# Performance work log

Measured on AMD Instinct MI355X. Metric: run time of the kernel, lower is better.

Reference implementation:

```python
import math
import jax, jax.numpy as jnp
import numpy as np

L_MAX = 3
PADDED = (1, 1, 2, 3)            # padded_l_list
K_MAX_L = (128, 96, 64, 32)      # channel bounds per l
FEATS = (32, 32, 32, 32)         # k_max_l[l] - k_max_l[l+1]
N_ATOMS = 20000
N_EDGES = 80000
N_RADIAL = 32
HIDDEN = 128
EPS = 1e-6


def setup_inputs() -> dict:
    key = jax.random.key(0)
    ks = jax.random.split(key, 40)
    it = iter(range(40))
    nk = lambda: ks[next(it)]
    inp = {}
    inp['rb'] = jax.random.normal(nk(), (L_MAX + 1, N_EDGES, N_RADIAL), jnp.float32)
    for l in range(L_MAX + 1):
        inp[f'sh{l}'] = jax.random.normal(nk(), (N_EDGES, 2 * l + 1), jnp.float32)
    for l in range(L_MAX + 1):
        P = PADDED[l]
        inp[f'f{l}'] = jax.random.normal(nk(), (N_ATOMS, P + 1, P + 1, FEATS[l]), jnp.float32)
    for P in (1, 2, 3):
        n = (P + 1) ** 2
        inp[f'U{P}'] = jax.random.normal(nk(), (n, n), jnp.float32) / math.sqrt(n)
    inp['gammas'] = jnp.ones((L_MAX + 1, 32), jnp.float32)
    inp['Win'] = jax.random.normal(nk(), (L_MAX + 1, 32, 32), jnp.float32) / math.sqrt(32.0)
    inp['Wout'] = jax.random.normal(nk(), (L_MAX + 1, 32, 32), jnp.float32) / math.sqrt(32.0)
    inp['A'] = jax.random.normal(nk(), (L_MAX + 1, N_RADIAL, HIDDEN), jnp.float32) / math.sqrt(float(N_RADIAL))
    for l in range(L_MAX + 1):
        inp[f'B{l}'] = jax.random.normal(nk(), (HIDDEN, K_MAX_L[l]), jnp.float32) / math.sqrt(float(HIDDEN))
    inp['msg_scale'] = jnp.float32(0.5)
    inp['centers'] = jax.random.randint(nk(), (N_EDGES,), 0, N_ATOMS)
    inp['neighbors'] = jax.random.randint(nk(), (N_EDGES,), 0, N_ATOMS)
    return inp


def _forward(rb, shs, feats, Us, gammas, Win, Wout, A, Bs, msg_scale, centers, neighbors):
    n_atoms = feats[0].shape[0]
    # EquivariantRMSNorm (norm over uncoupled i,j indices per channel) + linear_in
    h = []
    for l in range(L_MAX + 1):
        f = feats[l]
        rms = jnp.sqrt(jnp.mean(f * f, axis=(1, 2), keepdims=True) + EPS)
        fn = (f / rms) * gammas[l]
        h.append(jnp.einsum('nijf,fg->nijg', fn, Win[l]))
    # per-l radial MLP: [E, n_radial] -> silu -> [E, k_max_l[l]]
    rbm = [jax.nn.silu(rb[l] @ A[l]) @ Bs[l] for l in range(L_MAX + 1)]
    # vector expansion [E, 2l+1, k_max_l[l]]
    vexp = [shs[l][:, :, None] * rbm[l][:, None, :] for l in range(L_MAX + 1)]
    # split channels into per-l groups, uncouple via CG matrix U
    unc = []
    for l in range(L_MAX + 1):
        lower = K_MAX_L[l + 1] if l < L_MAX else 0
        upper = K_MAX_L[l]
        group = [vexp[lp][:, :, lower:upper] for lp in range(l + 1)]
        P = PADDED[l]
        if len(group) < P + 1:
            group.append(jnp.zeros((N_EDGES, 2 * P + 1, upper - lower), group[0].dtype))
        stacked = jnp.concatenate(group, axis=1)  # [E, (P+1)^2, feat]
        u = jnp.einsum('pq,eqf->epf', Us[P], stacked)
        unc.append(u.reshape(N_EDGES, P + 1, P + 1, upper - lower))
    # gather -> per-l tensor product -> scatter-add -> linear_out -> residual
    out = []
    for l in range(L_MAX + 1):
        P = PADDED[l]
        msg = jnp.einsum('eijf,ejkf->eikf', unc[l], h[l][neighbors]) / math.sqrt(P + 1.0)
        pooled = jnp.zeros((n_atoms,) + msg.shape[1:], msg.dtype).at[centers].add(msg) * msg_scale
        out.append(feats[l] + jnp.einsum('nijf,fg->nijg', pooled, Wout[l]))
    return tuple(out)


def reference(rb, sh0, sh1, sh2, sh3, f0, f1, f2, f3, U1, U2, U3, gammas, Win, Wout, A, B0, B1, B2, B3, msg_scale, centers, neighbors):
    return _forward(rb, [sh0, sh1, sh2, sh3], [f0, f1, f2, f3], {1: U1, 2: U2, 3: U3}, gammas, Win, Wout, A, [B0, B1, B2, B3], msg_scale, centers, neighbors)
```

## Files before the change

### kernel.cpp

```cpp
#include <hip/hip_runtime.h>
#include <cstdint>

#define NA 20000
#define NE 80000

typedef __attribute__((ext_vector_type(8))) short short8;
typedef __attribute__((ext_vector_type(4))) float f32x4;
typedef unsigned short ushort_t;

constexpr int HOFFc[4]   = {0, 2560000, 5120000, 10880000};
constexpr int RBMOFFc[4] = {0, 128, 224, 288};

__device__ __forceinline__ ushort_t f2bf(float x) {
    union { float f; unsigned u; } v; v.f = x;
    unsigned r = v.u + 0x7fffu + ((v.u >> 16) & 1u);
    return (ushort_t)(r >> 16);
}
__device__ __forceinline__ float bf2f(ushort_t u) {
    union { unsigned u; float f; } v; v.u = ((unsigned)u) << 16;
    return v.f;
}
__device__ __forceinline__ unsigned pack2(float a, float b) {
    return ((unsigned)f2bf(b) << 16) | (unsigned)f2bf(a);
}

__global__ __launch_bounds__(256)
void k_hist_prep(const int* __restrict__ centers, int* __restrict__ counts,
                 const float* __restrict__ B0, const float* __restrict__ B1,
                 const float* __restrict__ B2, const float* __restrict__ B3,
                 const float* __restrict__ A, const float* __restrict__ Win,
                 ushort_t* __restrict__ BT, ushort_t* __restrict__ ATb,
                 ushort_t* __restrict__ WinTb)
{
    const int b = blockIdx.x;
    if (b < 313) {
        const int e = b * 256 + threadIdx.x;
        if (e < NE) atomicAdd(&counts[centers[e]], 1);
        return;
    }
    const int i = (b - 313) * 256 + threadIdx.x;
    if (i < 40960) {
        const int n = i >> 7, k = i & 127;
        const float* src; int nl, N;
        if (n < 128)      { src = B0; nl = n;       N = 128; }
        else if (n < 224) { src = B1; nl = n - 128; N = 96;  }
        else if (n < 288) { src = B2; nl = n - 224; N = 64;  }
        else              { src = B3; nl = n - 288; N = 32;  }
        BT[i] = f2bf(src[k * N + nl]);
    } else if (i < 57344) {
        const int j2 = i - 40960;
        const int l = j2 >> 12, rem = j2 & 4095, jrow = rem >> 5, k = rem & 31;
        ATb[j2] = f2bf(A[l * 4096 + k * 128 + jrow]);
    } else if (i < 61440) {
        const int j3 = i - 57344;
        const int l = j3 >> 10, rem = j3 & 1023, g = rem >> 5, k = rem & 31;
        WinTb[j3] = f2bf(Win[l * 1024 + k * 32 + g]);
    }
}

template<int S, int AB>
__device__ __forceinline__ void norm_body(
    const float* __restrict__ fsel, const float* __restrict__ gammas, int l,
    const ushort_t* __restrict__ WinTb, ushort_t* __restrict__ hb,
    ushort_t* __restrict__ s_wt, float* __restrict__ s_scale)
{
    const int t = threadIdx.x;
    const int na0 = blockIdx.x * AB;

    if (t < 128) {
        reinterpret_cast<uint4*>(s_wt)[t] =
            reinterpret_cast<const uint4*>(WinTb + l * 1024)[t];
    }
    for (int i = t; i < AB * 32; i += 256) {
        const int a = i >> 5, c = i & 31;
        int aa = na0 + a; if (aa > NA - 1) aa = NA - 1;
        const float* fp = fsel + ((size_t)aa * S) * 32 + c;
        float ss = 0.f;
        #pragma unroll
        for (int s = 0; s < S; ++s) { const float v = fp[s * 32]; ss += v * v; }
        s_scale[i] = gammas[l * 32 + c] * rsqrtf(ss / (float)S + 1e-6f);
    }
    __syncthreads();

    const int w = t >> 6, lane = t & 63, l15 = lane & 15, lg = lane >> 4;
    const int row = w * 16 + l15;
    const bool rvalid = row < AB * S;
    const int rowc = rvalid ? row : 0;
    const int a = rowc / S, s = rowc % S;
    const int atom = na0 + a;
    const bool store_ok = rvalid && (atom < NA);
    const int atomc = (atom < NA) ? atom : (NA - 1);

    const float* fp = fsel + ((size_t)atomc * S + s) * 32 + lg * 8;
    const float4 x0 = *reinterpret_cast<const float4*>(fp);
    const float4 x1 = *reinterpret_cast<const float4*>(fp + 4);
    const float4 c0 = *reinterpret_cast<const float4*>(&s_scale[a * 32 + lg * 8]);
    const float4 c1 = *reinterpret_cast<const float4*>(&s_scale[a * 32 + lg * 8 + 4]);

    union { short8 v; unsigned u[4]; } bf;
    bf.u[0] = pack2(x0.x * c0.x, x0.y * c0.y);
    bf.u[1] = pack2(x0.z * c0.z, x0.w * c0.w);
    bf.u[2] = pack2(x1.x * c1.x, x1.y * c1.y);
    bf.u[3] = pack2(x1.z * c1.z, x1.w * c1.w);

    const short8 a0 = *reinterpret_cast<const short8*>(&s_wt[l15 * 32 + lg * 8]);
    const short8 a1 = *reinterpret_cast<const short8*>(&s_wt[(16 + l15) * 32 + lg * 8]);
    f32x4 d0 = __builtin_amdgcn_mfma_f32_16x16x32_bf16(a0, bf.v, (f32x4){0.f,0.f,0.f,0.f}, 0, 0, 0);
    f32x4 d1 = __builtin_amdgcn_mfma_f32_16x16x32_bf16(a1, bf.v, (f32x4){0.f,0.f,0.f,0.f}, 0, 0, 0);

    if (store_ok) {
        ushort_t* hp = hb + ((size_t)atomc * S + s) * 32;
        uint2 o0; o0.x = pack2(d0[0], d0[1]); o0.y = pack2(d0[2], d0[3]);
        uint2 o1; o1.x = pack2(d1[0], d1[1]); o1.y = pack2(d1[2], d1[3]);
        *reinterpret_cast<uint2*>(&hp[0  + 4 * lg]) = o0;
        *reinterpret_cast<uint2*>(&hp[16 + 4 * lg]) = o1;
    }
}

__global__ __launch_bounds__(256, 8)
void k_norm_mfma(const float* __restrict__ f0, const float* __restrict__ f1,
                 const float* __restrict__ f2, const float* __restrict__ f3,
                 const float* __restrict__ gammas, const ushort_t* __restrict__ WinTb,
                 ushort_t* __restrict__ h)
{
    __shared__ ushort_t s_wt[1024];
    __shared__ float s_scale[512];
    const int l = blockIdx.y;
    if (l == 0) {
        if (blockIdx.x >= 1250) return;
        norm_body<4, 16>(f0, gammas, 0, WinTb, h + HOFFc[0], s_wt, s_scale);
    } else if (l == 1) {
        if (blockIdx.x >= 1250) return;
        norm_body<4, 16>(f1, gammas, 1, WinTb, h + HOFFc[1], s_wt, s_scale);
    } else if (l == 2) {
        if (blockIdx.x >= 2858) return;
        norm_body<9, 7>(f2, gammas, 2, WinTb, h + HOFFc[2], s_wt, s_scale);
    } else {
        norm_body<16, 4>(f3, gammas, 3, WinTb, h + HOFFc[3], s_wt, s_scale);
    }
}

__global__ __launch_bounds__(256, 3)
void k_edgeA(const float* __restrict__ rb,
             const float* __restrict__ sh0, const float* __restrict__ sh1,
             const float* __restrict__ sh2, const float* __restrict__ sh3,
             const ushort_t* __restrict__ BT, const ushort_t* __restrict__ ATb,
             ushort_t* __restrict__ rbm, float* __restrict__ shq)
{
    __shared__ ushort_t s_h[8192];
    __shared__ ushort_t s_r2[16384];
    ushort_t* s_rbbf = s_r2;
    ushort_t* s_at   = s_r2 + 2048;
    ushort_t* s_bt   = s_r2;

    const int t  = threadIdx.x;
    const int e0 = blockIdx.x * 64;
    const int l  = blockIdx.y;
    const int w  = t >> 6, lane = t & 63;
    const int l15 = lane & 15, lg = lane >> 4;

    if (l == 0) {
        for (int i = t; i < 1024; i += 256) {
            const int q = i & 15, ge = e0 + (i >> 4);
            float v;
            if (q == 0)      v = sh0[ge];
            else if (q < 4)  v = sh1[ge * 3 + (q - 1)];
            else if (q < 9)  v = sh2[ge * 5 + (q - 4)];
            else             v = sh3[ge * 7 + (q - 9)];
            shq[(size_t)e0 * 16 + i] = v;
        }
    }

    const int Kl[4] = {128, 96, 64, 32};
    const int erow = w * 16 + l15;

    for (int i = t; i < 1024; i += 256) {
        const float2 v = *reinterpret_cast<const float2*>(
            &rb[(size_t)l * NE * 32 + (size_t)e0 * 32 + 2 * i]);
        *reinterpret_cast<unsigned*>(&s_rbbf[2 * i]) = pack2(v.x, v.y);
    }
    {
        const uint4* src = reinterpret_cast<const uint4*>(ATb + (size_t)l * 4096);
        for (int i = t; i < 512; i += 256) reinterpret_cast<uint4*>(s_at)[i] = src[i];
    }
    __syncthreads();

    const short8 rbf = *reinterpret_cast<const short8*>(&s_rbbf[erow * 32 + lg * 8]);
    #pragma unroll
    for (int jt = 0; jt < 8; ++jt) {
        const short8 af = *reinterpret_cast<const short8*>(&s_at[(jt * 16 + l15) * 32 + lg * 8]);
        f32x4 d = __builtin_amdgcn_mfma_f32_16x16x32_bf16(af, rbf, (f32x4){0.f,0.f,0.f,0.f}, 0, 0, 0);
        float s0 = d[0] / (1.f + __expf(-d[0]));
        float s1 = d[1] / (1.f + __expf(-d[1]));
        float s2 = d[2] / (1.f + __expf(-d[2]));
        float s3 = d[3] / (1.f + __expf(-d[3]));
        const int chunk = jt * 2 + (lg >> 1);
        const int base = erow * 128 + ((chunk ^ (erow & 7)) << 3) + (lg & 1) * 4;
        uint2 ov; ov.x = pack2(s0, s1); ov.y = pack2(s2, s3);
        *reinterpret_cast<uint2*>(&s_h[base]) = ov;
    }
    __syncthreads();

    const int K = Kl[l];
    for (int cch = t; cch < (K << 4); cch += 256) {
        const int n = cch >> 4, loc = cch & 15;
        const uint4 v = *reinterpret_cast<const uint4*>(&BT[(size_t)(RBMOFFc[l] + n) * 128 + loc * 8]);
        *reinterpret_cast<uint4*>(&s_bt[n * 128 + ((loc ^ (n & 7)) << 3)]) = v;
    }
    __syncthreads();

    const short8 hf0 = *reinterpret_cast<const short8*>(&s_h[erow * 128 + (((0 + lg) ^ (erow & 7)) << 3)]);
    const short8 hf1 = *reinterpret_cast<const short8*>(&s_h[erow * 128 + (((4 + lg) ^ (erow & 7)) << 3)]);
    const short8 hf2 = *reinterpret_cast<const short8*>(&s_h[erow * 128 + (((8 + lg) ^ (erow & 7)) << 3)]);
    const short8 hf3 = *reinterpret_cast<const short8*>(&s_h[erow * 128 + (((12 + lg) ^ (erow & 7)) << 3)]);

    const int ntn = K >> 4;
    for (int nt = 0; nt < ntn; ++nt) {
        const int n = nt * 16 + l15;
        f32x4 acc = {0.f, 0.f, 0.f, 0.f};
        #pragma unroll
        for (int ks = 0; ks < 4; ++ks) {
            const short8 af = *reinterpret_cast<const short8*>(
                &s_bt[n * 128 + (((ks * 4 + lg) ^ (n & 7)) << 3)]);
            const short8 hfk = (ks == 0) ? hf0 : (ks == 1) ? hf1 : (ks == 2) ? hf2 : hf3;
            acc = __builtin_amdgcn_mfma_f32_16x16x32_bf16(af, hfk, acc, 0, 0, 0);
        }
        uint2 ov;
        ov.x = pack2(acc[0], acc[1]);
        ov.y = pack2(acc[2], acc[3]);
        *reinterpret_cast<uint2*>(&rbm[(size_t)(e0 + erow) * 320 + RBMOFFc[l] + nt * 16 + 4 * lg]) = ov;
    }
}

__global__ __launch_bounds__(1024)
void k_scan(const int* __restrict__ counts, int* __restrict__ offsets)
{
    __shared__ int s_sum[1024];
    const int t = threadIdx.x;
    const int CH = 20;
    const int base = t * CH;
    int n = NA - base; n = n < 0 ? 0 : (n > CH ? CH : n);

    int tot = 0;
    for (int i = 0; i < n; i++) tot += counts[base + i];
    s_sum[t] = tot;
    __syncthreads();
    for (int off = 1; off < 1024; off <<= 1) {
        int v = (t >= off) ? s_sum[t - off] : 0;
        __syncthreads();
        s_sum[t] += v;
        __syncthreads();
    }
    int run = s_sum[t] - tot;
    for (int i = 0; i < n; i++) { offsets[base + i] = run; run += counts[base + i]; }
    if (t == 0) offsets[NA] = NE;
}

__global__ __launch_bounds__(256)
void k_fill(const int* __restrict__ centers, const int* __restrict__ offsets,
            int* __restrict__ cursor, int* __restrict__ elist)
{
    const int e = blockIdx.x * 256 + threadIdx.x;
    if (e < NE) {
        const int ctr = centers[e];
        const int pos = offsets[ctr] + atomicAdd(&cursor[ctr], 1);
        elist[pos] = e;
    }
}

template<int P1, int ASTART, int ACNT>
__device__ __forceinline__ void tp_step(float* __restrict__ acc,
                                        const float* __restrict__ lg,
                                        const ushort_t* __restrict__ lh,
                                        const float* __restrict__ rv, int c)
{
    float un[ACNT];
    #pragma unroll
    for (int pi = 0; pi < ACNT; ++pi) {
        const int p = ASTART + pi;
        float a = 0.f;
        #pragma unroll
        for (int lp = 0; lp < P1; ++lp) a += lg[p * 4 + lp] * rv[lp];
        un[pi] = a;
    }
    #pragma unroll
    for (int ii = 0; ii < ACNT / P1; ++ii) {
        #pragma unroll
        for (int k = 0; k < P1; ++k) {
            float m = 0.f;
            #pragma unroll
            for (int j = 0; j < P1; ++j) m += un[ii * P1 + j] * bf2f(lh[(j * P1 + k) * 32 + c]);
            acc[ii * P1 + k] += m;
        }
    }
}

template<int P1, int LOWER>
__device__ __forceinline__ void pool_big_body(
    const float* __restrict__ Up, float uscale,
    const float* __restrict__ WoutL, const float* __restrict__ msp,
    const float* __restrict__ shq, const ushort_t* __restrict__ rbm,
    const ushort_t* __restrict__ hL, const float* __restrict__ fL,
    float* __restrict__ outL,
    const int* __restrict__ offsets, const int* __restrict__ elist,
    const int* __restrict__ neighbors, float* __restrict__ sm)
{
    constexpr int S       = P1 * P1;
    constexpr int ACNT0   = (P1 == 4) ? 8 : 6;
    constexpr int ACNT1   = (P1 == 4) ? 8 : 3;
    constexpr int ASTART1 = ACNT0;
    constexpr int NV      = (S * 32) / 8;

    float*    s_U    = sm;
    float*    s_w    = sm + 256;
    ushort_t* s_hbuf = reinterpret_cast<ushort_t*>(sm + 256 + 1024);
    float*    s_gbuf = sm + 256 + 1024 + 64 * S;

    s_gbuf = sm + 256 + 1024 + 128 * S;

    const int t = threadIdx.x;
    for (int i = t; i < S * S; i += 256) s_U[i] = Up[i] * uscale;
    for (int i = t; i < 1024; i += 256) s_w[i] = WoutL[i];
    __syncthreads();

    const int w = t >> 6, lane = t & 63, c = lane & 31, half = lane >> 5;
    const int n = blockIdx.x * 4 + w;
    const float ms = *msp;
    const int beg = offsets[n], end = offsets[n + 1];

    const int gp = lane >> 2, glp = lane & 3;
    const int qlo = (glp == 0) ? 0 : (glp == 1) ? 1 : (glp == 2) ? 4 : 9;
    const int qhi = (glp == 0) ? 1 : (glp == 1) ? 4 : (glp == 2) ? 9 : 16;
    const bool gvalid = (gp < S) && (glp < P1);

    float acc[ACNT0];
    #pragma unroll
    for (int x = 0; x < ACNT0; ++x) acc[x] = 0.f;

    ushort_t* lhA = s_hbuf + w * 2 * (S * 32);
    ushort_t* lhB = lhA + S * 32;
    float*    lgA = s_gbuf + w * 128;
    float*    lgB = lgA + 64;

    for (int slot = beg; slot < end; slot += 2) {
        const bool haveB = (slot + 1) < end;
        const int eA = elist[slot];
        const int eB = elist[haveB ? slot + 1 : slot];
        const int nbrA = neighbors[eA];
        const int nbrB = neighbors[eB];

        uint4 vA = {}, vB = {};
        const uint4* hpA = reinterpret_cast<const uint4*>(hL + (size_t)nbrA * (S * 32));
        const uint4* hpB = reinterpret_cast<const uint4*>(hL + (size_t)nbrB * (S * 32));
        if (lane < NV) { vA = hpA[lane]; vB = hpB[lane]; }

        const ushort_t* rrA = rbm + (size_t)eA * 320 + LOWER + c;
        const ushort_t* rrB = rbm + (size_t)eB * 320 + LOWER + c;
        float rvA[4], rvB[4];
        #pragma unroll
        for (int lp = 0; lp < P1; ++lp) { rvA[lp] = bf2f(rrA[RBMOFFc[lp]]); rvB[lp] = bf2f(rrB[RBMOFFc[lp]]); }

        const float* sqA = shq + (size_t)eA * 16;
        const float* sqB = shq + (size_t)eB * 16;
        float gA = 0.f, gB = 0.f;
        if (gvalid) {
            for (int q = qlo; q < qhi; ++q) {
                const float u = s_U[gp * S + q];
                gA += u * sqA[q];
                gB += u * sqB[q];
            }
        }

        if (lane < NV) {
            reinterpret_cast<uint4*>(lhA)[lane] = vA;
            reinterpret_cast<uint4*>(lhB)[lane] = vB;
        }
        lgA[lane] = gA;
        lgB[lane] = gB;

        asm volatile("s_waitcnt lgkmcnt(0)" ::: "memory");

        if (half == 0) tp_step<P1, 0,       ACNT0>(acc, lgA, lhA, rvA, c);
        else           tp_step<P1, ASTART1, ACNT1>(acc, lgA, lhA, rvA, c);
        if (haveB) {
            if (half == 0) tp_step<P1, 0,       ACNT0>(acc, lgB, lhB, rvB, c);
            else           tp_step<P1, ASTART1, ACNT1>(acc, lgB, lhB, rvB, c);
        }
    }

    float* accStage = reinterpret_cast<float*>(lhA);
    if (half == 0) {
        #pragma unroll
        for (int x = 0; x < ACNT0; ++x) accStage[x * 32 + c] = acc[x];
    } else {
        #pragma unroll
        for (int x = 0; x < ACNT1; ++x) accStage[(ASTART1 + x) * 32 + c] = acc[x];
    }
    asm volatile("s_waitcnt lgkmcnt(0)" ::: "memory");

    const float* fp = fL + (size_t)n * (S * 32);
    float* op = outL + (size_t)n * (S * 32);
    for (int s = half; s < S; s += 2) {
        float o = 0.f;
        #pragma unroll
        for (int f = 0; f < 32; f++) o += accStage[s * 32 + f] * s_w[f * 32 + c];
        op[s * 32 + c] = fp[s * 32 + c] + ms * o;
    }
}

__device__ __forceinline__ void pool_01_body(
    const float* __restrict__ U1, const float* __restrict__ Wout,
    const float* __restrict__ msp, const float* __restrict__ shq,
    const ushort_t* __restrict__ rbm, const ushort_t* __restrict__ h,
    const float* __restrict__ f0, const float* __restrict__ f1,
    float* __restrict__ out,
    const int* __restrict__ offsets, const int* __restrict__ elist,
    const int* __restrict__ neighbors, float* __restrict__ sm)
{
    float* s_U   = sm;
    float* s_w   = sm + 16;
    float* s_acc = sm + 16 + 2048;

    const int t = threadIdx.x;
    if (t < 16) s_U[t] = U1[t] * 0.70710678118654752f;
    for (int i = t; i < 2048; i += 256) s_w[i] = Wout[i];
    __syncthreads();

    const int w = t >> 6, lane = t & 63, c = lane & 31, half = lane >> 5;
    const int n = blockIdx.x * 4 + w;
    const float ms = *msp;
    const int beg = offsets[n], end = offsets[n + 1];
    const ushort_t* h0 = h;
    const ushort_t* h1 = h + 2560000;

    float acc0[4] = {0.f, 0.f, 0.f, 0.f};
    float acc1[4] = {0.f, 0.f, 0.f, 0.f};

    const int nit = (end - beg + 1) >> 1;
    for (int it = 0; it < nit; ++it) {
        const int slot = beg + it * 2 + half;
        const bool valid = slot < end;
        const int e   = elist[valid ? slot : beg];
        const int nbr = neighbors[e];
        const float fac = valid ? 1.f : 0.f;

        const ushort_t* rrow = rbm + (size_t)e * 320;
        const float rv0  = fac * bf2f(rrow[96 + c]);
        const float rv1a = fac * bf2f(rrow[64 + c]);
        const float rv1b = fac * bf2f(rrow[192 + c]);
        const float* sqp = shq + (size_t)e * 16;
        const float sq0 = sqp[0], sq1 = sqp[1], sq2 = sqp[2], sq3 = sqp[3];

        float hn0[4], hn1[4];
        const ushort_t* hp0 = h0 + (size_t)nbr * 128 + c;
        const ushort_t* hp1 = h1 + (size_t)nbr * 128 + c;
        #pragma unroll
        for (int p = 0; p < 4; ++p) { hn0[p] = bf2f(hp0[p * 32]); hn1[p] = bf2f(hp1[p * 32]); }

        const float st0 = sq0 * rv0;
        float st1[4];
        st1[0] = sq0 * rv1a; st1[1] = sq1 * rv1b; st1[2] = sq2 * rv1b; st1[3] = sq3 * rv1b;

        float unc0[4], unc1[4];
        #pragma unroll
        for (int p = 0; p < 4; ++p) {
            unc0[p] = s_U[p * 4] * st0;
            float a = 0.f;
            #pragma unroll
            for (int q = 0; q < 4; ++q) a += s_U[p * 4 + q] * st1[q];
            unc1[p] = a;
        }
        #pragma unroll
        for (int i = 0; i < 2; ++i) {
            #pragma unroll
            for (int k = 0; k < 2; ++k) {
                float m0 = 0.f, m1 = 0.f;
                #pragma unroll
                for (int j = 0; j < 2; ++j) {
                    m0 += unc0[i * 2 + j] * hn0[j * 2 + k];
                    m1 += unc1[i * 2 + j] * hn1[j * 2 + k];
                }
                acc0[i * 2 + k] += m0;
                acc1[i * 2 + k] += m1;
            }
        }
    }

    #pragma unroll
    for (int s = 0; s < 4; s++) { acc0[s] += __shfl_xor(acc0[s], 32); acc1[s] += __shfl_xor(acc1[s], 32); }
    #pragma unroll
    for (int s = 0; s < 4; s++) if ((s & 1) == half) {
        s_acc[(w * 2 + 0) * 128 + s * 32 + c] = acc0[s];
        s_acc[(w * 2 + 1) * 128 + s * 32 + c] = acc1[s];
    }
    __syncthreads();

    const float* fp0 = f0 + (size_t)n * 128;
    const float* fp1 = f1 + (size_t)n * 128;
    float* op0 = out + (size_t)n * 128;
    float* op1 = out + 2560000 + (size_t)n * 128;
    for (int s = half; s < 4; s += 2) {
        float o0 = 0.f, o1 = 0.f;
        #pragma unroll
        for (int f = 0; f < 32; f++) {
            o0 += s_acc[(w * 2 + 0) * 128 + s * 32 + f] * s_w[f * 32 + c];
            o1 += s_acc[(w * 2 + 1) * 128 + s * 32 + f] * s_w[1024 + f * 32 + c];
        }
        op0[s * 32 + c] = fp0[s * 32 + c] + ms * o0;
        op1[s * 32 + c] = fp1[s * 32 + c] + ms * o1;
    }
}

__global__ __launch_bounds__(256, 6)
void k_pools(const float* __restrict__ U1, const float* __restrict__ U2,
             const float* __restrict__ U3, const float* __restrict__ Wout,
             const float* __restrict__ msp, const float* __restrict__ shq,
             const ushort_t* __restrict__ rbm, const ushort_t* __restrict__ h,
             const float* __restrict__ f0, const float* __restrict__ f1,
             const float* __restrict__ f2, const float* __restrict__ f3,
             float* __restrict__ out,
             const int* __restrict__ offsets, const int* __restrict__ elist,
             const int* __restrict__ neighbors)
{
    __shared__ float sm[3840];
    const int which = blockIdx.y;
    if (which == 0) {
        pool_big_body<4, 0>(U3, 0.5f, Wout + 3072, msp, shq, rbm,
                            h + HOFFc[3], f3, out + HOFFc[3],
                            offsets, elist, neighbors, sm);
    } else if (which == 1) {
        pool_big_body<3, 32>(U2, 0.57735026918962576f, Wout + 2048, msp, shq, rbm,
                             h + HOFFc[2], f2, out + HOFFc[2],
                             offsets, elist, neighbors, sm);
    } else {
        pool_01_body(U1, Wout, msp, shq, rbm, h, f0, f1, out,
                     offsets, elist, neighbors, sm);
    }
}

extern "C" void kernel_launch(void* const* d_in, const int* in_sizes, int n_in,
                              void* d_out, int out_size, void* d_ws, size_t ws_size,
                              hipStream_t stream)
{
    (void)in_sizes; (void)n_in; (void)out_size;

    const float* rb     = (const float*)d_in[0];
    const float* sh0    = (const float*)d_in[1];
    const float* sh1    = (const float*)d_in[2];
    const float* sh2    = (const float*)d_in[3];
    const float* sh3    = (const float*)d_in[4];
    const float* f0     = (const float*)d_in[5];
    const float* f1     = (const float*)d_in[6];
    const float* f2     = (const float*)d_in[7];
    const float* f3     = (const float*)d_in[8];
    const float* U1     = (const float*)d_in[9];
    const float* U2     = (const float*)d_in[10];
    const float* U3     = (const float*)d_in[11];
    const float* gammas = (const float*)d_in[12];
    const float* Win    = (const float*)d_in[13];
    const float* Wout   = (const float*)d_in[14];
    const float* A      = (const float*)d_in[15];
    const float* B0     = (const float*)d_in[16];
    const float* B1     = (const float*)d_in[17];
    const float* B2     = (const float*)d_in[18];
    const float* B3     = (const float*)d_in[19];
    const float* msp    = (const float*)d_in[20];
    const int* centers   = (const int*)d_in[21];
    const int* neighbors = (const int*)d_in[22];

    const size_t OFF_RBM = 42240000;
    const size_t OFF_SHQ = 93440000;
    const size_t OFF_BT  = 98560000;
    const size_t OFF_AT  = 98641920;
    const size_t OFF_WT  = 98674688;
    const size_t OFF_INT = 98682880;
    const size_t needed  = OFF_INT + (size_t)140001 * 4;
    if (ws_size < needed) return;

    ushort_t* h_bf  = (ushort_t*)d_ws;
    ushort_t* rbm   = (ushort_t*)((char*)d_ws + OFF_RBM);
    float*    shq   = (float*)((char*)d_ws + OFF_SHQ);
    ushort_t* BT    = (ushort_t*)((char*)d_ws + OFF_BT);
    ushort_t* ATb   = (ushort_t*)((char*)d_ws + OFF_AT);
    ushort_t* WinTb = (ushort_t*)((char*)d_ws + OFF_WT);
    int* ibase   = (int*)((char*)d_ws + OFF_INT);
    int* offsets = ibase;
    int* counts  = ibase + 20001;
    int* cursor  = ibase + 40001;
    int* elist   = ibase + 60001;

    hipMemsetAsync(counts, 0, (size_t)40000 * sizeof(int), stream);

    k_hist_prep<<<553, 256, 0, stream>>>(centers, counts, B0, B1, B2, B3, A, Win,
                                         BT, ATb, WinTb);
    k_scan<<<1, 1024, 0, stream>>>(counts, offsets);
    k_fill<<<313, 256, 0, stream>>>(centers, offsets, cursor, elist);

    dim3 gN(5000, 4);
    k_norm_mfma<<<gN, 256, 0, stream>>>(f0, f1, f2, f3, gammas, WinTb, h_bf);
    dim3 gE(1250, 4);
    k_edgeA<<<gE, 256, 0, stream>>>(rb, sh0, sh1, sh2, sh3, BT, ATb, rbm, shq);

    dim3 gP(5000, 3);
    k_pools<<<gP, 256, 0, stream>>>(U1, U2, U3, Wout, msp, shq, rbm, h_bf,
                                    f0, f1, f2, f3, (float*)d_out,
                                    offsets, elist, neighbors);
}
```

Measured before the change: 282.3 us.

## Merge norm and edge-MLP kernels into one launch, raise pool occupancy bound

Combines the independent norm and edge radial-MLP kernels into a single kernel with a flattened 1D grid. The first 5000 blocks do edge work and the rest do the per-l norm, with shared memory overlaid between the two roles. This removes one launch and drops the wasted early-exit blocks the old 2D norm grid had. The merged kernel keeps the edge kernel's launch bound of 3, so norm blocks may run at lower occupancy than before. The pool kernel's launch-bounds occupancy hint is raised from 6 to 8, which may force register spills.

```diff
diff --git a/kernel.cpp b/kernel.cpp
--- a/kernel.cpp
+++ b/kernel.cpp
@@ -60,12 +60,12 @@
 
 template<int S, int AB>
 __device__ __forceinline__ void norm_body(
-    const float* __restrict__ fsel, const float* __restrict__ gammas, int l,
+    int bx, const float* __restrict__ fsel, const float* __restrict__ gammas, int l,
     const ushort_t* __restrict__ WinTb, ushort_t* __restrict__ hb,
     ushort_t* __restrict__ s_wt, float* __restrict__ s_scale)
 {
     const int t = threadIdx.x;
-    const int na0 = blockIdx.x * AB;
+    const int na0 = bx * AB;
 
     if (t < 128) {
         reinterpret_cast<uint4*>(s_wt)[t] =
@@ -117,46 +117,23 @@
     }
 }
 
-__global__ __launch_bounds__(256, 8)
-void k_norm_mfma(const float* __restrict__ f0, const float* __restrict__ f1,
-                 const float* __restrict__ f2, const float* __restrict__ f3,
-                 const float* __restrict__ gammas, const ushort_t* __restrict__ WinTb,
-                 ushort_t* __restrict__ h)
-{
-    __shared__ ushort_t s_wt[1024];
-    __shared__ float s_scale[512];
-    const int l = blockIdx.y;
-    if (l == 0) {
-        if (blockIdx.x >= 1250) return;
-        norm_body<4, 16>(f0, gammas, 0, WinTb, h + HOFFc[0], s_wt, s_scale);
-    } else if (l == 1) {
-        if (blockIdx.x >= 1250) return;
-        norm_body<4, 16>(f1, gammas, 1, WinTb, h + HOFFc[1], s_wt, s_scale);
-    } else if (l == 2) {
-        if (blockIdx.x >= 2858) return;
-        norm_body<9, 7>(f2, gammas, 2, WinTb, h + HOFFc[2], s_wt, s_scale);
-    } else {
-        norm_body<16, 4>(f3, gammas, 3, WinTb, h + HOFFc[3], s_wt, s_scale);
-    }
-}
-
-__global__ __launch_bounds__(256, 3)
-void k_edgeA(const float* __restrict__ rb,
-             const float* __restrict__ sh0, const float* __restrict__ sh1,
-             const float* __restrict__ sh2, const float* __restrict__ sh3,
-             const ushort_t* __restrict__ BT, const ushort_t* __restrict__ ATb,
-             ushort_t* __restrict__ rbm, float* __restrict__ shq)
-{
-    __shared__ ushort_t s_h[8192];
-    __shared__ ushort_t s_r2[16384];
+__device__ __forceinline__ void edge_body(
+    int l, int e0,
+    const float* __restrict__ rb,
+    const float* __restrict__ sh0, const float* __restrict__ sh1,
+    const float* __restrict__ sh2, const float* __restrict__ sh3,
+    const ushort_t* __restrict__ BT, const ushort_t* __restrict__ ATb,
+    ushort_t* __restrict__ rbm, float* __restrict__ shq,
+    ushort_t* __restrict__ smem)
+{
+    ushort_t* s_h  = smem;
+    ushort_t* s_r2 = smem + 8192;
     ushort_t* s_rbbf = s_r2;
     ushort_t* s_at   = s_r2 + 2048;
     ushort_t* s_bt   = s_r2;
 
-    const int t  = threadIdx.x;
-    const int e0 = blockIdx.x * 64;
-    const int l  = blockIdx.y;
-    const int w  = t >> 6, lane = t & 63;
+    const int t = threadIdx.x;
+    const int w = t >> 6, lane = t & 63;
     const int l15 = lane & 15, lg = lane >> 4;
 
     if (l == 0) {
@@ -232,6 +209,34 @@
     }
 }
 
+__global__ __launch_bounds__(256, 3)
+void k_ne(const float* __restrict__ rb,
+          const float* __restrict__ sh0, const float* __restrict__ sh1,
+          const float* __restrict__ sh2, const float* __restrict__ sh3,
+          const float* __restrict__ f0, const float* __restrict__ f1,
+          const float* __restrict__ f2, const float* __restrict__ f3,
+          const float* __restrict__ gammas,
+          const ushort_t* __restrict__ BT, const ushort_t* __restrict__ ATb,
+          const ushort_t* __restrict__ WinTb,
+          ushort_t* __restrict__ rbm, float* __restrict__ shq,
+          ushort_t* __restrict__ h)
+{
+    __shared__ ushort_t smem[24576];
+    const int b = blockIdx.x;
+    if (b < 5000) {
+        edge_body(b / 1250, (b % 1250) * 64, rb, sh0, sh1, sh2, sh3,
+                  BT, ATb, rbm, shq, smem);
+        return;
+    }
+    ushort_t* s_wt   = smem;
+    float*    s_scale = reinterpret_cast<float*>(smem + 1024);
+    const int nb = b - 5000;
+    if (nb < 1250)       norm_body<4, 16>(nb,        f0, gammas, 0, WinTb, h + HOFFc[0], s_wt, s_scale);
+    else if (nb < 2500)  norm_body<4, 16>(nb - 1250, f1, gammas, 1, WinTb, h + HOFFc[1], s_wt, s_scale);
+    else if (nb < 5358)  norm_body<9, 7>(nb - 2500,  f2, gammas, 2, WinTb, h + HOFFc[2], s_wt, s_scale);
+    else                 norm_body<16, 4>(nb - 5358, f3, gammas, 3, WinTb, h + HOFFc[3], s_wt, s_scale);
+}
+
 __global__ __launch_bounds__(1024)
 void k_scan(const int* __restrict__ counts, int* __restrict__ offsets)
 {
@@ -314,9 +319,7 @@
     float*    s_U    = sm;
     float*    s_w    = sm + 256;
     ushort_t* s_hbuf = reinterpret_cast<ushort_t*>(sm + 256 + 1024);
-    float*    s_gbuf = sm + 256 + 1024 + 64 * S;
-
-    s_gbuf = sm + 256 + 1024 + 128 * S;
+    float*    s_gbuf = sm + 256 + 1024 + 128 * S;
 
     const int t = threadIdx.x;
     for (int i = t; i < S * S; i += 256) s_U[i] = Up[i] * uscale;
@@ -511,7 +514,7 @@
     }
 }
 
-__global__ __launch_bounds__(256, 6)
+__global__ __launch_bounds__(256, 8)
 void k_pools(const float* __restrict__ U1, const float* __restrict__ U2,
              const float* __restrict__ U3, const float* __restrict__ Wout,
              const float* __restrict__ msp, const float* __restrict__ shq,
@@ -596,10 +599,8 @@
     k_scan<<<1, 1024, 0, stream>>>(counts, offsets);
     k_fill<<<313, 256, 0, stream>>>(centers, offsets, cursor, elist);
 
-    dim3 gN(5000, 4);
-    k_norm_mfma<<<gN, 256, 0, stream>>>(f0, f1, f2, f3, gammas, WinTb, h_bf);
-    dim3 gE(1250, 4);
-    k_edgeA<<<gE, 256, 0, stream>>>(rb, sh0, sh1, sh2, sh3, BT, ATb, rbm, shq);
+    k_ne<<<15358, 256, 0, stream>>>(rb, sh0, sh1, sh2, sh3, f0, f1, f2, f3,
+                                    gammas, BT, ATb, WinTb, rbm, shq, h_bf);
 
     dim3 gP(5000, 3);
     k_pools<<<gP, 256, 0, stream>>>(U1, U2, U3, Wout, msp, shq, rbm, h_bf,
```

New measurement: 322.5 us. 1.14x slower.
